# Performance work log

Hardware: AMD Instinct MI355X
Metric: run time of the kernel (lower is better)

## Reference

```python
import jax, jax.numpy as jnp
import numpy as np

NUM_ITEMS = 100000
OUT_DIM = 128
BATCH = 16384
HIST = 50
TOTAL = BATCH * HIST


def setup_inputs() -> dict:
    key = jax.random.key(0)
    k1, k2, k3, k4, k5, k6 = jax.random.split(key, 6)
    feature_ids = jax.random.randint(k1, (TOTAL,), 0, NUM_ITEMS + 1, dtype=jnp.int64 if jax.config.jax_enable_x64 else jnp.int32)
    # ratings in {0.5, 1.0, ..., 5.0} so that (r - 0.5) * 2 is an int index in [0, 10)
    ratings = jax.random.randint(k2, (TOTAL,), 0, 10).astype(jnp.float32) / 2.0 + 0.5
    segment_ids = jnp.repeat(jnp.arange(BATCH, dtype=jnp.int32), HIST)  # [TOTAL]
    item_ids = jax.random.randint(k3, (BATCH,), 0, NUM_ITEMS, dtype=jnp.int32)
    # kaiming_uniform_(a=sqrt(5)) on an [N, D] table -> U(-b, b) with b = sqrt(6 / ((1 + 5) * D)) = 1/sqrt(D)
    b = 1.0 / np.sqrt(OUT_DIM)
    user_W = jax.random.uniform(k4, (NUM_ITEMS + 1, OUT_DIM), jnp.float32, -b, b)
    rating_W = jax.random.uniform(k5, (10, OUT_DIM), jnp.float32, -b, b)
    item_W = jax.random.uniform(k6, (NUM_ITEMS, OUT_DIM), jnp.float32, -b, b)
    bias = jnp.zeros((OUT_DIM,), jnp.float32)
    return {"feature_ids": feature_ids, "ratings": ratings, "segment_ids": segment_ids,
            "item_ids": item_ids, "user_W": user_W, "rating_W": rating_W,
            "item_W": item_W, "bias": bias}


def reference(feature_ids, ratings, segment_ids, item_ids, user_W, rating_W, item_W, bias):
    batch = item_ids.shape[0]
    rating_idx = ((ratings - 0.5) * 2.0).astype(jnp.int32)          # [T], in [0, 10)
    rating_weights = rating_W[rating_idx]                            # [T, D] gather
    user_weights = user_W[feature_ids] * rating_weights              # [T, D] gather + multiply
    user_sum = jax.ops.segment_sum(user_weights, segment_ids, num_segments=batch)  # [B, D]
    return user_sum + item_W[item_ids] + bias                        # [B, D]
```

## Files before the change

kernel.cpp:

```cpp
#include <hip/hip_runtime.h>


#define BATCH     16384
#define HIST      50
#define TOTAL     (BATCH * HIST)
#define UNROLL    10
#define DIM4      32
#define NROWS_U   100001
#define SLICES    8
#define SL_H4     (NROWS_U * 4)
#define UT_H4     (SLICES * SL_H4)
#define UT_BYTES  ((size_t)UT_H4 * 8)
#define RPB       64
#define BLOCK     256

struct __attribute__((aligned(8))) half4 { _Float16 x, y, z, w; };

__global__ __launch_bounds__(256) void convert_pack_kernel(
    const float4* __restrict__ src,
    const int*    __restrict__ feature_ids,
    const float*  __restrict__ ratings,
    half4*        __restrict__ uT,
    int*          __restrict__ packed)
{
    const int tid = blockIdx.x * 256 + threadIdx.x;
    const int stride = gridDim.x * 256;
    if (blockIdx.y < SLICES) {
        const int slice = blockIdx.y;
        half4* dst = uT + (size_t)slice * SL_H4;
        for (int i = tid; i < SL_H4; i += stride) {
            const int row = i >> 2, d = i & 3;
            const float4 v = src[row * DIM4 + slice * 4 + d];
            half4 h;
            h.x = (_Float16)v.x; h.y = (_Float16)v.y;
            h.z = (_Float16)v.z; h.w = (_Float16)v.w;
            dst[i] = h;
        }
    } else {
        for (int t = tid; t < TOTAL; t += stride) {
            const int fid  = feature_ids[t];
            const int ridx = (int)(ratings[t] * 2.0f) - 1;
            packed[t] = (fid << 4) | ridx;
        }
    }
}

__global__ __launch_bounds__(BLOCK) void features_linear_sliced(
    const int*    __restrict__ packed,
    const int*    __restrict__ item_ids,
    const half4*  __restrict__ uT,
    const float4* __restrict__ rating_W,
    const float4* __restrict__ item_W,
    const float4* __restrict__ bias,
    float4*       __restrict__ out)
{
    __shared__ int    sh_pid[RPB * HIST];
    __shared__ float4 sh_rW[10 * 4];

    const int tid   = threadIdx.x;
    const int slice = blockIdx.x & 7;
    const int grp   = blockIdx.x >> 3;

    if (tid < 40)
        sh_rW[tid] = rating_W[(tid >> 2) * DIM4 + slice * 4 + (tid & 3)];

    const int base = grp * (RPB * HIST);
    for (int i = tid; i < RPB * HIST; i += BLOCK)
        sh_pid[i] = packed[base + i];
    __syncthreads();

    const int row = tid >> 2;
    const int d   = tid & 3;
    const int b   = grp * RPB + row;
    const int off = row * HIST;

    const half4* us = uT + (size_t)slice * SL_H4;

    float4 acc; acc.x = 0.f; acc.y = 0.f; acc.z = 0.f; acc.w = 0.f;

    for (int h = 0; h < HIST; h += UNROLL) {
        int p[UNROLL];
#pragma unroll
        for (int i = 0; i < UNROLL; ++i) p[i] = sh_pid[off + h + i];

        half4 u[UNROLL];
#pragma unroll
        for (int i = 0; i < UNROLL; ++i)
            u[i] = us[(p[i] >> 4) * 4 + d];

#pragma unroll
        for (int i = 0; i < UNROLL; ++i) {
            const float4 w = sh_rW[(p[i] & 15) * 4 + d];
            acc.x += (float)u[i].x * w.x;
            acc.y += (float)u[i].y * w.y;
            acc.z += (float)u[i].z * w.z;
            acc.w += (float)u[i].w * w.w;
        }
    }

    const int    iid = item_ids[b];
    const float4 iw  = item_W[iid * DIM4 + slice * 4 + d];
    const float4 bs  = bias[slice * 4 + d];

    float4 o;
    o.x = acc.x + iw.x + bs.x;
    o.y = acc.y + iw.y + bs.y;
    o.z = acc.z + iw.z + bs.z;
    o.w = acc.w + iw.w + bs.w;
    out[b * DIM4 + slice * 4 + d] = o;
}

__global__ __launch_bounds__(BLOCK) void features_linear_f32(
    const int*    __restrict__ feature_ids,
    const float*  __restrict__ ratings,
    const int*    __restrict__ item_ids,
    const float4* __restrict__ user_W,
    const float4* __restrict__ rating_W,
    const float4* __restrict__ item_W,
    const float4* __restrict__ bias,
    float4*       __restrict__ out)
{
    __shared__ float4 sh_rW[10 * DIM4];
    __shared__ int    sh_fid[8 * HIST];
    __shared__ int    sh_ridx[8 * HIST];

    const int tid = threadIdx.x;
    for (int i = tid; i < 10 * DIM4; i += BLOCK) sh_rW[i] = rating_W[i];
    const int base = blockIdx.x * (8 * HIST);
    for (int i = tid; i < 8 * HIST; i += BLOCK) {
        sh_fid[i] = feature_ids[base + i];
        float r = ratings[base + i];
        sh_ridx[i] = (int)(r * 2.0f) - 1;
    }
    __syncthreads();

    const int row = tid >> 5;
    const int d4  = tid & 31;
    const int b   = blockIdx.x * 8 + row;

    float4 acc; acc.x = 0.f; acc.y = 0.f; acc.z = 0.f; acc.w = 0.f;
    const int off = row * HIST;

    for (int h = 0; h < HIST; h += UNROLL) {
        int f[UNROLL], r[UNROLL];
#pragma unroll
        for (int i = 0; i < UNROLL; ++i) {
            f[i] = sh_fid[off + h + i];
            r[i] = sh_ridx[off + h + i];
        }
        float4 u[UNROLL];
#pragma unroll
        for (int i = 0; i < UNROLL; ++i) u[i] = user_W[f[i] * DIM4 + d4];
#pragma unroll
        for (int i = 0; i < UNROLL; ++i) {
            const float4 w = sh_rW[r[i] * DIM4 + d4];
            acc.x += u[i].x * w.x;
            acc.y += u[i].y * w.y;
            acc.z += u[i].z * w.z;
            acc.w += u[i].w * w.w;
        }
    }

    const int    iid = item_ids[b];
    const float4 iw  = item_W[iid * DIM4 + d4];
    const float4 bs  = bias[d4];

    float4 o;
    o.x = acc.x + iw.x + bs.x;
    o.y = acc.y + iw.y + bs.y;
    o.z = acc.z + iw.z + bs.z;
    o.w = acc.w + iw.w + bs.w;
    out[b * DIM4 + d4] = o;
}

extern "C" void kernel_launch(void* const* d_in, const int* in_sizes, int n_in,
                              void* d_out, int out_size, void* d_ws, size_t ws_size,
                              hipStream_t stream) {
    const int*    feature_ids = (const int*)   d_in[0];
    const float*  ratings     = (const float*) d_in[1];
    const int*    item_ids    = (const int*)   d_in[3];
    const float4* user_W      = (const float4*)d_in[4];
    const float4* rating_W    = (const float4*)d_in[5];
    const float4* item_W      = (const float4*)d_in[6];
    const float4* bias        = (const float4*)d_in[7];
    float4*       out         = (float4*)      d_out;

    const size_t need = UT_BYTES + (size_t)TOTAL * sizeof(int);
    if (d_ws != nullptr && ws_size >= need) {
        half4* uT     = (half4*)d_ws;
        int*   packed = (int*)((char*)d_ws + UT_BYTES);

        convert_pack_kernel<<<dim3(784, 9), dim3(256), 0, stream>>>(
            user_W, feature_ids, ratings, uT, packed);

        features_linear_sliced<<<dim3((BATCH / RPB) * SLICES), dim3(BLOCK), 0, stream>>>(
            packed, item_ids, uT, rating_W, item_W, bias, out);
    } else {
        features_linear_f32<<<dim3(BATCH / 8), dim3(BLOCK), 0, stream>>>(
            feature_ids, ratings, item_ids, user_W, rating_W, item_W, bias, out);
    }
}
```

Before: 174.6 us.

## Widen sliced fp16 gathers to 16-byte loads with four column slices

Reorganizes the fp16 transposed user table into 4 slices of 32 columns, so each thread gathers 8 halves in one 16-byte load instead of 4 halves in an 8-byte load. Halving the slice count halves the gather block count and the redundant packed-id and rating-table loads per slice. It also adds a padded shared rating table, an asm barrier that forces all ten loads to issue before use, and a launch-bounds occupancy hint. The cost is more registers per thread (eight accumulators and wider loaded values), and each slice of the table now spans a larger working set.

```diff
diff --git a/kernel.cpp b/kernel.cpp
--- a/kernel.cpp
+++ b/kernel.cpp
@@ -7,34 +7,37 @@
 #define UNROLL    10
 #define DIM4      32
 #define NROWS_U   100001
-#define SLICES    8
-#define SL_H4     (NROWS_U * 4)
-#define UT_H4     (SLICES * SL_H4)
-#define UT_BYTES  ((size_t)UT_H4 * 8)
+#define SLICES    4
+#define SL_U4     (NROWS_U * 4)
+#define UT_BYTES  ((size_t)SLICES * SL_U4 * 16)
 #define RPB       64
 #define BLOCK     256
-
-struct __attribute__((aligned(8))) half4 { _Float16 x, y, z, w; };
+#define RWPAD     36
+
+typedef unsigned int u32x4 __attribute__((ext_vector_type(4)));
 
 __global__ __launch_bounds__(256) void convert_pack_kernel(
     const float4* __restrict__ src,
     const int*    __restrict__ feature_ids,
     const float*  __restrict__ ratings,
-    half4*        __restrict__ uT,
+    u32x4*        __restrict__ uT,
     int*          __restrict__ packed)
 {
     const int tid = blockIdx.x * 256 + threadIdx.x;
     const int stride = gridDim.x * 256;
     if (blockIdx.y < SLICES) {
         const int slice = blockIdx.y;
-        half4* dst = uT + (size_t)slice * SL_H4;
-        for (int i = tid; i < SL_H4; i += stride) {
-            const int row = i >> 2, d = i & 3;
-            const float4 v = src[row * DIM4 + slice * 4 + d];
-            half4 h;
-            h.x = (_Float16)v.x; h.y = (_Float16)v.y;
-            h.z = (_Float16)v.z; h.w = (_Float16)v.w;
-            dst[i] = h;
+        u32x4* dst = uT + (size_t)slice * SL_U4;
+        for (int i = tid; i < SL_U4; i += stride) {
+            const int row = i >> 2, q = i & 3;
+            const float4 a = src[row * DIM4 + slice * 8 + q * 2];
+            const float4 b = src[row * DIM4 + slice * 8 + q * 2 + 1];
+            union { u32x4 v; _Float16 h[8]; } o;
+            o.h[0] = (_Float16)a.x; o.h[1] = (_Float16)a.y;
+            o.h[2] = (_Float16)a.z; o.h[3] = (_Float16)a.w;
+            o.h[4] = (_Float16)b.x; o.h[5] = (_Float16)b.y;
+            o.h[6] = (_Float16)b.z; o.h[7] = (_Float16)b.w;
+            dst[i] = o.v;
         }
     } else {
         for (int t = tid; t < TOTAL; t += stride) {
@@ -45,24 +48,26 @@
     }
 }
 
-__global__ __launch_bounds__(BLOCK) void features_linear_sliced(
+__global__ __launch_bounds__(BLOCK, 4) void features_linear_sliced(
     const int*    __restrict__ packed,
     const int*    __restrict__ item_ids,
-    const half4*  __restrict__ uT,
-    const float4* __restrict__ rating_W,
+    const u32x4*  __restrict__ uT,
+    const float*  __restrict__ rating_Wf,
     const float4* __restrict__ item_W,
     const float4* __restrict__ bias,
     float4*       __restrict__ out)
 {
-    __shared__ int    sh_pid[RPB * HIST];
-    __shared__ float4 sh_rW[10 * 4];
+    __shared__ int   sh_pid[RPB * HIST];
+    __shared__ float sh_rW[10 * RWPAD];
 
     const int tid   = threadIdx.x;
-    const int slice = blockIdx.x & 7;
-    const int grp   = blockIdx.x >> 3;
-
-    if (tid < 40)
-        sh_rW[tid] = rating_W[(tid >> 2) * DIM4 + slice * 4 + (tid & 3)];
+    const int slice = blockIdx.x & 3;
+    const int grp   = blockIdx.x >> 2;
+
+    for (int i = tid; i < 10 * 32; i += BLOCK) {
+        const int r = i >> 5, j = i & 31;
+        sh_rW[r * RWPAD + j] = rating_Wf[r * 128 + slice * 32 + j];
+    }
 
     const int base = grp * (RPB * HIST);
     for (int i = tid; i < RPB * HIST; i += BLOCK)
@@ -70,44 +75,65 @@
     __syncthreads();
 
     const int row = tid >> 2;
-    const int d   = tid & 3;
+    const int q   = tid & 3;
     const int b   = grp * RPB + row;
     const int off = row * HIST;
 
-    const half4* us = uT + (size_t)slice * SL_H4;
-
-    float4 acc; acc.x = 0.f; acc.y = 0.f; acc.z = 0.f; acc.w = 0.f;
+    const u32x4* us = uT + (size_t)slice * SL_U4;
+
+    float a0 = 0.f, a1 = 0.f, a2 = 0.f, a3 = 0.f,
+          a4 = 0.f, a5 = 0.f, a6 = 0.f, a7 = 0.f;
 
     for (int h = 0; h < HIST; h += UNROLL) {
-        int p[UNROLL];
-#pragma unroll
-        for (int i = 0; i < UNROLL; ++i) p[i] = sh_pid[off + h + i];
-
-        half4 u[UNROLL];
-#pragma unroll
-        for (int i = 0; i < UNROLL; ++i)
-            u[i] = us[(p[i] >> 4) * 4 + d];
-
-#pragma unroll
-        for (int i = 0; i < UNROLL; ++i) {
-            const float4 w = sh_rW[(p[i] & 15) * 4 + d];
-            acc.x += (float)u[i].x * w.x;
-            acc.y += (float)u[i].y * w.y;
-            acc.z += (float)u[i].z * w.z;
-            acc.w += (float)u[i].w * w.w;
-        }
+        const int p0 = sh_pid[off + h + 0], p1 = sh_pid[off + h + 1];
+        const int p2 = sh_pid[off + h + 2], p3 = sh_pid[off + h + 3];
+        const int p4 = sh_pid[off + h + 4], p5 = sh_pid[off + h + 5];
+        const int p6 = sh_pid[off + h + 6], p7 = sh_pid[off + h + 7];
+        const int p8 = sh_pid[off + h + 8], p9 = sh_pid[off + h + 9];
+
+        u32x4 u0 = us[(p0 >> 4) * 4 + q];
+        u32x4 u1 = us[(p1 >> 4) * 4 + q];
+        u32x4 u2 = us[(p2 >> 4) * 4 + q];
+        u32x4 u3 = us[(p3 >> 4) * 4 + q];
+        u32x4 u4 = us[(p4 >> 4) * 4 + q];
+        u32x4 u5 = us[(p5 >> 4) * 4 + q];
+        u32x4 u6 = us[(p6 >> 4) * 4 + q];
+        u32x4 u7 = us[(p7 >> 4) * 4 + q];
+        u32x4 u8 = us[(p8 >> 4) * 4 + q];
+        u32x4 u9 = us[(p9 >> 4) * 4 + q];
+
+        asm volatile("" : "+v"(u0), "+v"(u1), "+v"(u2), "+v"(u3), "+v"(u4),
+                          "+v"(u5), "+v"(u6), "+v"(u7), "+v"(u8), "+v"(u9));
+
+#define CONSUME(uk, pk)                                                  \
+        {                                                                \
+            union { u32x4 v; _Float16 hh[8]; } c; c.v = uk;              \
+            const float* w = &sh_rW[(pk & 15) * RWPAD + q * 8];          \
+            a0 += (float)c.hh[0] * w[0]; a1 += (float)c.hh[1] * w[1];    \
+            a2 += (float)c.hh[2] * w[2]; a3 += (float)c.hh[3] * w[3];    \
+            a4 += (float)c.hh[4] * w[4]; a5 += (float)c.hh[5] * w[5];    \
+            a6 += (float)c.hh[6] * w[6]; a7 += (float)c.hh[7] * w[7];    \
+        }
+        CONSUME(u0, p0) CONSUME(u1, p1) CONSUME(u2, p2) CONSUME(u3, p3)
+        CONSUME(u4, p4) CONSUME(u5, p5) CONSUME(u6, p6) CONSUME(u7, p7)
+        CONSUME(u8, p8) CONSUME(u9, p9)
+#undef CONSUME
     }
 
     const int    iid = item_ids[b];
-    const float4 iw  = item_W[iid * DIM4 + slice * 4 + d];
-    const float4 bs  = bias[slice * 4 + d];
-
-    float4 o;
-    o.x = acc.x + iw.x + bs.x;
-    o.y = acc.y + iw.y + bs.y;
-    o.z = acc.z + iw.z + bs.z;
-    o.w = acc.w + iw.w + bs.w;
-    out[b * DIM4 + slice * 4 + d] = o;
+    const int    e   = slice * 8 + q * 2;
+    const float4 iw0 = item_W[iid * DIM4 + e];
+    const float4 iw1 = item_W[iid * DIM4 + e + 1];
+    const float4 bs0 = bias[e];
+    const float4 bs1 = bias[e + 1];
+
+    float4 o0, o1;
+    o0.x = a0 + iw0.x + bs0.x; o0.y = a1 + iw0.y + bs0.y;
+    o0.z = a2 + iw0.z + bs0.z; o0.w = a3 + iw0.w + bs0.w;
+    o1.x = a4 + iw1.x + bs1.x; o1.y = a5 + iw1.y + bs1.y;
+    o1.z = a6 + iw1.z + bs1.z; o1.w = a7 + iw1.w + bs1.w;
+    out[b * DIM4 + e]     = o0;
+    out[b * DIM4 + e + 1] = o1;
 }
 
 __global__ __launch_bounds__(BLOCK) void features_linear_f32(
@@ -187,14 +213,14 @@
 
     const size_t need = UT_BYTES + (size_t)TOTAL * sizeof(int);
     if (d_ws != nullptr && ws_size >= need) {
-        half4* uT     = (half4*)d_ws;
+        u32x4* uT     = (u32x4*)d_ws;
         int*   packed = (int*)((char*)d_ws + UT_BYTES);
 
-        convert_pack_kernel<<<dim3(784, 9), dim3(256), 0, stream>>>(
+        convert_pack_kernel<<<dim3(784, 5), dim3(256), 0, stream>>>(
             user_W, feature_ids, ratings, uT, packed);
 
         features_linear_sliced<<<dim3((BATCH / RPB) * SLICES), dim3(BLOCK), 0, stream>>>(
-            packed, item_ids, uT, rating_W, item_W, bias, out);
+            packed, item_ids, uT, (const float*)rating_W, item_W, bias, out);
     } else {
         features_linear_f32<<<dim3(BATCH / 8), dim3(BLOCK), 0, stream>>>(
             feature_ids, ratings, item_ids, user_W, rating_W, item_W, bias, out);
```

New measurement: 167.9 us. 1.04x faster.
